# Performance work log

Measured on AMD Instinct MI355X. Metric: run time of the kernel, lower is better.

The kernel has to match this reference:

```python
import jax, jax.numpy as jnp
import numpy as np

BS = 64; T = 96; C = 16; IN = 16; H = 256; NH = 8; DH = H // NH
NCLS = 4; L = T + NCLS; LAYERS = 4; GDEP = 2; EPS = 1e-5


def _ln(x, g, b):
    m = x.mean(-1, keepdims=True)
    v = ((x - m) ** 2).mean(-1, keepdims=True)
    return (x - m) / jnp.sqrt(v + EPS) * g + b


def _mask():
    # causal upper-triangular -inf mask; last NCLS rows (cls tokens) attend everywhere
    m = jnp.where(jnp.triu(jnp.ones((L, L), jnp.float32), 1) > 0, -jnp.inf, 0.0)
    return m.at[-NCLS:].set(0.0)


def _enc(h, mask, Wqkv, bqkv, Wo, bo, W1, b1, W2, b2, g1, be1, g2, be2):
    # post-norm TransformerEncoderLayer (torch default), dropout=0
    B = h.shape[0]
    qkv = h @ Wqkv.T + bqkv
    q, k, v = jnp.split(qkv, 3, axis=-1)
    sp = lambda t: t.reshape(B, L, NH, DH).transpose(0, 2, 1, 3)
    q, k, v = sp(q), sp(k), sp(v)
    s = jnp.einsum('bhqd,bhkd->bhqk', q, k) / np.float32(np.sqrt(DH)) + mask
    a = jax.nn.softmax(s, axis=-1)
    o = jnp.einsum('bhqk,bhkd->bhqd', a, v).transpose(0, 2, 1, 3).reshape(B, L, H)
    h = _ln(h + o @ Wo.T + bo, g1, be1)
    ff = jax.nn.relu(h @ W1.T + b1) @ W2.T + b2
    return _ln(h + ff, g2, be2)


def _mixprop(x, g, Wm, bm):
    # x: (bs, H, C, NCLS); MTGNN mixprop with alpha=0
    adj = g + jnp.eye(C, dtype=g.dtype)
    a = adj / adj.sum(1, keepdims=True)
    h = x
    outs = [x]
    for _ in range(GDEP):
        h = jnp.einsum('ncwl,vw->ncvl', h, a)
        outs.append(h)
    ho = jnp.concatenate(outs, axis=1)  # (bs, (GDEP+1)*H, C, NCLS)
    return jnp.einsum('ncwl,oc->nowl', ho, Wm) + bm[None, :, None, None]


def _forward(x, Wfc, bfc, cls_token, pos_emb, emb1, emb2, Wl1, bl1, Wl2, bl2,
             Wqkv, bqkv, Wo, bo, W1, b1, W2, b2, ln1g, ln1b, ln2g, ln2b,
             Wmlp, bmlp, Wd1, bd1, Wd2, bd2):
    bs = x.shape[0]
    h = x @ Wfc.T + bfc                                      # (bs,T,C,H)
    h = jnp.concatenate([h, jnp.broadcast_to(cls_token, (bs, NCLS, C, H))], axis=1)
    h = h + pos_emb[None]                                    # (bs,L,C,H)
    h = jnp.swapaxes(h, 1, 2).reshape(bs * C, L, H)
    mask = _mask()
    # graph_constructor (alpha=1)
    m1 = jnp.tanh(emb1 @ Wl1.T + bl1)
    m2 = jnp.tanh(emb2 @ Wl2.T + bl2)
    g = jax.nn.relu(jnp.tanh(m1 @ m2.T - m2 @ m1.T))         # (C,C)
    h = _enc(h, mask, Wqkv[0], bqkv[0], Wo[0], bo[0], W1[0], b1[0], W2[0], b2[0],
             ln1g[0], ln1b[0], ln2g[0], ln2b[0])
    for l in range(1, LAYERS):
        cls = h[:, -NCLS:].reshape(bs, C, NCLS, H).transpose(0, 3, 1, 2)  # (bs,H,C,NCLS)
        cls = _mixprop(cls, g, Wmlp[l - 1], bmlp[l - 1])
        cls = cls.transpose(0, 2, 3, 1).reshape(bs * C, NCLS, H)
        h = jnp.concatenate([h[:, :-NCLS], cls], axis=1)
        h = _enc(h, mask, Wqkv[l], bqkv[l], Wo[l], bo[l], W1[l], b1[l], W2[l], b2[l],
                 ln1g[l], ln1b[l], ln2g[l], ln2b[l])
    z = jnp.tanh(h[:, -NCLS:].reshape(bs, C * NCLS * H))
    z = jax.nn.gelu(z @ Wd1.T + bd1, approximate=False) @ Wd2.T + bd2
    return z[:, 0]


def setup_inputs() -> dict:
    key = jax.random.key(0)
    ks = iter(jax.random.split(key, 64))
    rn = lambda *s: jax.random.normal(next(ks), s, dtype=jnp.float32) * 0.05
    d = {}
    d['x'] = jax.random.normal(next(ks), (BS, T, C, IN), dtype=jnp.float32)
    d['p'] = jnp.zeros((BS,), jnp.float32)
    d['y'] = jnp.zeros((BS,), jnp.float32)
    d['Wfc'] = rn(H, IN); d['bfc'] = jnp.zeros((H,), jnp.float32)
    d['cls_token'] = rn(1, NCLS, C, H) * 20.0  # torch randn scale ~1
    d['pos_emb'] = rn(NCLS + T, C, H) * 20.0
    d['emb1'] = rn(C, H); d['emb2'] = rn(C, H)
    d['Wl1'] = rn(H, H); d['bl1'] = jnp.zeros((H,), jnp.float32)
    d['Wl2'] = rn(H, H); d['bl2'] = jnp.zeros((H,), jnp.float32)
    d['Wqkv'] = rn(LAYERS, 3 * H, H); d['bqkv'] = jnp.zeros((LAYERS, 3 * H), jnp.float32)
    d['Wo'] = rn(LAYERS, H, H); d['bo'] = jnp.zeros((LAYERS, H), jnp.float32)
    d['W1'] = rn(LAYERS, 4 * H, H); d['b1'] = jnp.zeros((LAYERS, 4 * H), jnp.float32)
    d['W2'] = rn(LAYERS, H, 4 * H); d['b2'] = jnp.zeros((LAYERS, H), jnp.float32)
    d['ln1g'] = jnp.ones((LAYERS, H), jnp.float32); d['ln1b'] = jnp.zeros((LAYERS, H), jnp.float32)
    d['ln2g'] = jnp.ones((LAYERS, H), jnp.float32); d['ln2b'] = jnp.zeros((LAYERS, H), jnp.float32)
    d['Wmlp'] = rn(LAYERS - 1, H, (GDEP + 1) * H); d['bmlp'] = jnp.zeros((LAYERS - 1, H), jnp.float32)
    d['Wd1'] = rn(H, NCLS * C * H); d['bd1'] = jnp.zeros((H,), jnp.float32)
    d['Wd2'] = rn(1, H); d['bd2'] = jnp.zeros((1,), jnp.float32)
    return d


def reference(x, p, y, Wfc, bfc, cls_token, pos_emb, emb1, emb2, Wl1, bl1, Wl2, bl2,
              Wqkv, bqkv, Wo, bo, W1, b1, W2, b2, ln1g, ln1b, ln2g, ln2b,
              Wmlp, bmlp, Wd1, bd1, Wd2, bd2):
    # p, y are unused by the original forward (kept for signature parity)
    return _forward(x, Wfc, bfc, cls_token, pos_emb, emb1, emb2, Wl1, bl1, Wl2, bl2,
                    Wqkv, bqkv, Wo, bo, W1, b1, W2, b2, ln1g, ln1b, ln2g, ln2b,
                    Wmlp, bmlp, Wd1, bd1, Wd2, bd2)
```

## Files before the change

### kernel.cpp

```cpp
#include <hip/hip_runtime.h>
#include <hip/hip_bf16.h>
#include <math.h>

typedef unsigned short u16;
typedef unsigned int   u32;
typedef __attribute__((ext_vector_type(8))) short short8;
typedef __attribute__((ext_vector_type(4))) float f32x4;

#define BSZ   64
#define TT    96
#define CCH   16
#define INDIM 16
#define HD    256
#define NHEAD 8
#define DHEAD 32
#define NCLS  4
#define LSEQ  100
#define NLAY  4
#define EPSV  1e-5f
#define BSEQ  (BSZ*CCH)
#define MTOK  (BSEQ*LSEQ)

__device__ __forceinline__ float bf2f(u16 x){ return __uint_as_float(((u32)x)<<16); }
__device__ __forceinline__ u16 f2bf(float f){
    u32 u = __float_as_uint(f);
    u32 r = (u + 0x7fffu + ((u>>16)&1u)) >> 16;
    return (u16)r;
}
__device__ __forceinline__ float lo16(u32 r){ return __uint_as_float(r<<16); }
__device__ __forceinline__ float hi16(u32 r){ return __uint_as_float(r&0xffff0000u); }

__device__ __forceinline__ u32 cvtpk(float lo, float hi){
    u32 r;
    asm("v_cvt_pk_bf16_f32 %0, %1, %2" : "=v"(r) : "v"(lo), "v"(hi));
    return r;
}

__device__ __forceinline__ void gload_lds16(const u16* g, u16* l){
    __builtin_amdgcn_global_load_lds(
        (const __attribute__((address_space(1))) unsigned int*)g,
        (__attribute__((address_space(3))) unsigned int*)l, 16, 0, 0);
}

__global__ __launch_bounds__(256)
void k_cvt(const float* __restrict__ src, u16* __restrict__ dst, int n)
{
    for (int i = blockIdx.x*256 + threadIdx.x; i < n; i += gridDim.x*256)
        dst[i] = f2bf(src[i]);
}

__global__ __launch_bounds__(256)
void k_embed(const float* __restrict__ x, const float* __restrict__ Wfc,
             const float* __restrict__ bfc, const float* __restrict__ cls,
             const float* __restrict__ pos, u16* __restrict__ h)
{
    int s = blockIdx.x;
    int n = s >> 4, c = s & 15;
    int hc = threadIdx.x;
    float wr[INDIM];
    #pragma unroll
    for (int i=0;i<INDIM;i++) wr[i] = Wfc[hc*INDIM + i];
    float bb = bfc[hc];
    for (int l=0; l<TT; l++){
        const float* xr = x + (size_t)((n*TT + l)*CCH + c)*INDIM;
        float acc = bb;
        #pragma unroll
        for (int i=0;i<INDIM;i++) acc += xr[i]*wr[i];
        acc += pos[(size_t)(l*CCH + c)*HD + hc];
        h[((size_t)s*LSEQ + l)*HD + hc] = f2bf(acc);
    }
    #pragma unroll
    for (int l=TT; l<LSEQ; l++){
        float v = cls[(size_t)((l-TT)*CCH + c)*HD + hc]
                + pos[(size_t)(l*CCH + c)*HD + hc];
        h[((size_t)s*LSEQ + l)*HD + hc] = f2bf(v);
    }
}

__global__ __launch_bounds__(256)
void k_graph_m(const float* __restrict__ emb, const float* __restrict__ Wl,
               const float* __restrict__ bl, float* __restrict__ m)
{
    int r = blockIdx.x, o = threadIdx.x;
    __shared__ float e[HD];
    e[o] = emb[r*HD + o];
    __syncthreads();
    const float* w = Wl + (size_t)o*HD;
    float acc = bl[o];
    for (int k=0;k<HD;k++) acc += e[k]*w[k];
    m[r*HD + o] = tanhf(acc);
}

__global__ __launch_bounds__(256)
void k_graph_a(const float* __restrict__ m1, const float* __restrict__ m2,
               float* __restrict__ a)
{
    int t = threadIdx.x; int v = t >> 4, w = t & 15;
    __shared__ float adj[16][17];
    float s1=0.f, s2=0.f;
    for (int k=0;k<HD;k++){
        s1 += m1[v*HD+k]*m2[w*HD+k];
        s2 += m2[v*HD+k]*m1[w*HD+k];
    }
    float g = tanhf(s1 - s2); g = g > 0.f ? g : 0.f;
    adj[v][w] = g + (v==w ? 1.f : 0.f);
    __syncthreads();
    float rs = 0.f;
    #pragma unroll
    for (int j=0;j<16;j++) rs += adj[v][j];
    a[t] = adj[v][w] / rs;
}

__global__ __launch_bounds__(256)
void k_gemmA(const u16* __restrict__ A, int lda,
             const u16* __restrict__ W, const float* __restrict__ bias,
             u16* __restrict__ C, int ldc, int K, int relu, int scat)
{
    __shared__ u16 smem[32768];
    u16* As0 = smem;
    u16* As1 = smem + 8192;
    u16* Ws0 = smem + 16384;
    u16* Ws1 = smem + 24576;

    int t = threadIdx.x;
    int lane = t & 63, w = t >> 6;
    int wm = (w & 1)*64, wn = (w >> 1)*64;
    int fr = lane & 15, quad = lane >> 4;

    int nwg = gridDim.x * gridDim.y;
    int bid = blockIdx.y * gridDim.x + blockIdx.x;
    int tile = bid;
    if (!(nwg & 7)){
        int cpx = nwg >> 3;
        tile = (bid & 7)*cpx + (bid >> 3);
    }
    int bx = tile % gridDim.x, by = tile / gridDim.x;
    size_t mb = (size_t)by * 128;
    int nb = bx * 128;

    int srow = lane >> 2;
    int sslot = lane & 3;

    f32x4 acc[4][4] = {};

    auto STAGE = [&](int bb, int k0){
        #pragma unroll
        for (int i=0;i<2;i++){
            int r = w*32 + i*16 + srow;
            int cw = sslot ^ ((r>>1)&3);
            gload_lds16(&A[(mb + r)*(size_t)lda + k0      + cw*8], &As0[bb*4096 + (w*32 + i*16)*32]);
            gload_lds16(&A[(mb + r)*(size_t)lda + k0 + 32 + cw*8], &As1[bb*4096 + (w*32 + i*16)*32]);
            gload_lds16(&W[(size_t)(nb + r)*K   + k0      + cw*8], &Ws0[bb*4096 + (w*32 + i*16)*32]);
            gload_lds16(&W[(size_t)(nb + r)*K   + k0 + 32 + cw*8], &Ws1[bb*4096 + (w*32 + i*16)*32]);
        }
    };
    auto COMPUTE = [&](int bb){
        short8 af0[4], af1[4], bf0[4], bf1[4];
        #pragma unroll
        for (int mt=0; mt<4; mt++){
            int r = wm + mt*16 + fr;
            int sw = (quad ^ ((r>>1)&3)) << 3;
            af0[mt] = *(const short8*)&As0[bb*4096 + r*32 + sw];
            af1[mt] = *(const short8*)&As1[bb*4096 + r*32 + sw];
        }
        #pragma unroll
        for (int nt=0; nt<4; nt++){
            int r = wn + nt*16 + fr;
            int sw = (quad ^ ((r>>1)&3)) << 3;
            bf0[nt] = *(const short8*)&Ws0[bb*4096 + r*32 + sw];
            bf1[nt] = *(const short8*)&Ws1[bb*4096 + r*32 + sw];
        }
        #pragma unroll
        for (int mt=0; mt<4; mt++)
            #pragma unroll
            for (int nt=0; nt<4; nt++){
                acc[mt][nt] = __builtin_amdgcn_mfma_f32_16x16x32_bf16(
                    af0[mt], bf0[nt], acc[mt][nt], 0, 0, 0);
                acc[mt][nt] = __builtin_amdgcn_mfma_f32_16x16x32_bf16(
                    af1[mt], bf1[nt], acc[mt][nt], 0, 0, 0);
            }
    };

    const int nst = K >> 6;
    STAGE(0, 0);
    asm volatile("s_waitcnt vmcnt(0)" ::: "memory");
    __builtin_amdgcn_s_barrier();
    int b = 0;
    for (int ts = 0; ts < nst; ++ts){
        if (ts + 1 < nst) STAGE(b^1, (ts+1) << 6);
        COMPUTE(b);
        asm volatile("s_waitcnt vmcnt(0)" ::: "memory");
        __builtin_amdgcn_s_barrier();
        b ^= 1;
    }

    float bb4[4];
    #pragma unroll
    for (int nt=0; nt<4; nt++) bb4[nt] = bias[nb + wn + nt*16 + fr];
    __syncthreads();
    u16* Ct = smem;
    #pragma unroll
    for (int mt=0; mt<4; mt++){
        int rw = wm + mt*16 + quad*4;
        #pragma unroll
        for (int nt=0; nt<4; nt++){
            int col = wn + nt*16 + fr;
            float v0 = acc[mt][nt][0] + bb4[nt];
            float v1 = acc[mt][nt][1] + bb4[nt];
            float v2 = acc[mt][nt][2] + bb4[nt];
            float v3 = acc[mt][nt][3] + bb4[nt];
            if (relu){
                v0 = v0 > 0.f ? v0 : 0.f;  v1 = v1 > 0.f ? v1 : 0.f;
                v2 = v2 > 0.f ? v2 : 0.f;  v3 = v3 > 0.f ? v3 : 0.f;
            }
            u32 p01 = cvtpk(v0, v1), p23 = cvtpk(v2, v3);
            Ct[(rw+0)*128 + col] = (u16)p01;
            Ct[(rw+1)*128 + col] = (u16)(p01 >> 16);
            Ct[(rw+2)*128 + col] = (u16)p23;
            Ct[(rw+3)*128 + col] = (u16)(p23 >> 16);
        }
    }
    __syncthreads();
    #pragma unroll
    for (int it=0; it<8; ++it){
        int row = it*16 + (t>>4);
        int seg = t & 15;
        size_t rg = mb + row;
        if (scat) rg = (rg >> 2)*LSEQ + TT + (rg & 3);
        *(short8*)&C[rg*(size_t)ldc + nb + seg*8] = *(const short8*)&Ct[row*128 + seg*8];
    }
}

__global__ __launch_bounds__(256)
void k_gemmC(const u16* __restrict__ A, int lda, int K,
             const u16* __restrict__ W, const float* __restrict__ bias,
             u16* __restrict__ h, const float* __restrict__ gam,
             const float* __restrict__ bet, size_t row0)
{
    __shared__ u16 smem[40960];
    u16* As0 = smem;
    u16* As1 = smem + 4096;
    u16* Ws0 = smem + 8192;
    u16* Ws1 = smem + 24576;

    int t = threadIdx.x;
    int lane = t & 63, w = t >> 6;
    int fr = lane & 15, quad = lane >> 4;
    size_t mb = (size_t)blockIdx.x * 64;
    int srow = lane >> 2, sslot = lane & 3;

    f32x4 acc[4][4] = {};

    auto STAGE = [&](int bb, int k0){
        {
            int r = w*16 + srow;
            int cw = sslot ^ ((r>>1)&3);
            gload_lds16(&A[(mb + r)*(size_t)lda + k0      + cw*8], &As0[bb*2048 + (w*16)*32]);
            gload_lds16(&A[(mb + r)*(size_t)lda + k0 + 32 + cw*8], &As1[bb*2048 + (w*16)*32]);
        }
        #pragma unroll
        for (int i=0;i<4;i++){
            int r = w*64 + i*16 + srow;
            int cw = sslot ^ ((r>>1)&3);
            gload_lds16(&W[(size_t)r*K + k0      + cw*8], &Ws0[bb*8192 + (w*64 + i*16)*32]);
            gload_lds16(&W[(size_t)r*K + k0 + 32 + cw*8], &Ws1[bb*8192 + (w*64 + i*16)*32]);
        }
    };
    auto COMPUTE = [&](int bb){
        short8 af0[4], af1[4], bf0[4], bf1[4];
        #pragma unroll
        for (int mt=0; mt<4; mt++){
            int ra = mt*16 + fr;
            int swa = (quad ^ ((ra>>1)&3)) << 3;
            af0[mt] = *(const short8*)&As0[bb*2048 + ra*32 + swa];
            af1[mt] = *(const short8*)&As1[bb*2048 + ra*32 + swa];
        }
        #pragma unroll
        for (int nt=0; nt<4; nt++){
            int rb = w*64 + nt*16 + fr;
            int swb = (quad ^ ((rb>>1)&3)) << 3;
            bf0[nt] = *(const short8*)&Ws0[bb*8192 + rb*32 + swb];
            bf1[nt] = *(const short8*)&Ws1[bb*8192 + rb*32 + swb];
        }
        #pragma unroll
        for (int mt=0; mt<4; mt++)
            #pragma unroll
            for (int nt=0; nt<4; nt++){
                acc[mt][nt] = __builtin_amdgcn_mfma_f32_16x16x32_bf16(
                    af0[mt], bf0[nt], acc[mt][nt], 0, 0, 0);
                acc[mt][nt] = __builtin_amdgcn_mfma_f32_16x16x32_bf16(
                    af1[mt], bf1[nt], acc[mt][nt], 0, 0, 0);
            }
    };

    const int nst = K >> 6;
    STAGE(0, 0);
    asm volatile("s_waitcnt vmcnt(0)" ::: "memory");
    __builtin_amdgcn_s_barrier();
    int b = 0;
    for (int ts = 0; ts < nst; ++ts){
        if (ts + 1 < nst) STAGE(b^1, (ts+1) << 6);
        COMPUTE(b);
        asm volatile("s_waitcnt vmcnt(0)" ::: "memory");
        __builtin_amdgcn_s_barrier();
        b ^= 1;
    }

    float bb4[4], gg[4], be[4];
    #pragma unroll
    for (int nt=0; nt<4; nt++){
        int col = w*64 + nt*16 + fr;
        bb4[nt] = bias[col]; gg[nt] = gam[col]; be[nt] = bet[col];
    }
    #pragma unroll
    for (int mt=0; mt<4; mt++){
        #pragma unroll
        for (int r=0; r<4; r++){
            size_t row = row0 + mb + mt*16 + quad*4 + r;
            #pragma unroll
            for (int nt=0; nt<4; nt++)
                acc[mt][nt][r] += bb4[nt] + bf2f(h[row*HD + w*64 + nt*16 + fr]);
        }
    }
    __syncthreads();
    float* red  = (float*)smem;
    float* red2 = (float*)(smem + 512);
    float ps[4][4];
    #pragma unroll
    for (int mt=0; mt<4; mt++)
        #pragma unroll
        for (int r=0; r<4; r++){
            float s = acc[mt][0][r] + acc[mt][1][r] + acc[mt][2][r] + acc[mt][3][r];
            s += __shfl_xor(s,1,64); s += __shfl_xor(s,2,64);
            s += __shfl_xor(s,4,64); s += __shfl_xor(s,8,64);
            ps[mt][r] = s;
        }
    if (fr == 0){
        #pragma unroll
        for (int mt=0; mt<4; mt++)
            #pragma unroll
            for (int r=0; r<4; r++)
                red[w*64 + mt*16 + quad*4 + r] = ps[mt][r];
    }
    __syncthreads();
    float mean[4][4];
    #pragma unroll
    for (int mt=0; mt<4; mt++)
        #pragma unroll
        for (int r=0; r<4; r++){
            int rl = mt*16 + quad*4 + r;
            mean[mt][r] = (red[rl] + red[64+rl] + red[128+rl] + red[192+rl]) * (1.f/256.f);
            float s = 0.f;
            #pragma unroll
            for (int nt=0; nt<4; nt++){ float d = acc[mt][nt][r] - mean[mt][r]; s += d*d; }
            s += __shfl_xor(s,1,64); s += __shfl_xor(s,2,64);
            s += __shfl_xor(s,4,64); s += __shfl_xor(s,8,64);
            ps[mt][r] = s;
        }
    if (fr == 0){
        #pragma unroll
        for (int mt=0; mt<4; mt++)
            #pragma unroll
            for (int r=0; r<4; r++)
                red2[w*64 + mt*16 + quad*4 + r] = ps[mt][r];
    }
    __syncthreads();
    u16* Ct = smem + 8192;
    #pragma unroll
    for (int mt=0; mt<4; mt++)
        #pragma unroll
        for (int r=0; r<4; r++){
            int rl = mt*16 + quad*4 + r;
            float inv = rsqrtf((red2[rl] + red2[64+rl] + red2[128+rl] + red2[192+rl])
                               * (1.f/256.f) + EPSV);
            float o0 = (acc[mt][0][r] - mean[mt][r]) * inv * gg[0] + be[0];
            float o1 = (acc[mt][1][r] - mean[mt][r]) * inv * gg[1] + be[1];
            float o2 = (acc[mt][2][r] - mean[mt][r]) * inv * gg[2] + be[2];
            float o3 = (acc[mt][3][r] - mean[mt][r]) * inv * gg[3] + be[3];
            u32 p01 = cvtpk(o0, o1), p23 = cvtpk(o2, o3);
            Ct[rl*256 + w*64 +  0 + fr] = (u16)p01;
            Ct[rl*256 + w*64 + 16 + fr] = (u16)(p01 >> 16);
            Ct[rl*256 + w*64 + 32 + fr] = (u16)p23;
            Ct[rl*256 + w*64 + 48 + fr] = (u16)(p23 >> 16);
        }
    __syncthreads();
    #pragma unroll
    for (int it=0; it<8; ++it){
        int row = it*8 + (t>>5);
        int seg = t & 31;
        *(short8*)&h[(row0 + mb + row)*HD + seg*8] = *(const short8*)&Ct[row*256 + seg*8];
    }
}

#define KS_STR 40
#define VT_STR 136
#define PL_STR 136
__global__ __launch_bounds__(256)
void k_attn(u16* __restrict__ qkv)
{
    __shared__ u16 smem[26368];
    int t = threadIdx.x;
    int w = t >> 6, lane = t & 63;
    int fr = lane & 15, quad = lane >> 4;
    int p = t >> 7, t2 = t & 127;
    u16* Ks = smem + p*4480;
    u16* Vt = smem + 8960 + p*4352;
    u16* Pl = smem + 17664 + w*2176;

    {
        int gp = blockIdx.x*2 + p;
        size_t base = (size_t)(gp >> 3)*LSEQ*768 + (gp & 7)*32;
        for (int idx = t2; idx < 1792; idx += 128){
            int key = idx >> 4, d2 = (idx & 15) << 1;
            u32 kv = (key < LSEQ) ? *(const u32*)&qkv[base + (size_t)key*768 + 256 + d2] : 0u;
            *(u32*)&Ks[key*KS_STR + d2] = kv;
        }
        for (int idx = t2; idx < 2048; idx += 128){
            int key = idx >> 4, d2 = (idx & 15) << 1;
            u32 vv = (key < LSEQ) ? *(const u32*)&qkv[base + (size_t)key*768 + 512 + d2] : 0u;
            Vt[ d2   *VT_STR + key] = (u16)(vv & 0xffffu);
            Vt[(d2+1)*VT_STR + key] = (u16)(vv >> 16);
        }
    }
    __syncthreads();

    int wp = w >> 1;
    int gp = blockIdx.x*2 + wp;
    size_t base = (size_t)(gp >> 3)*LSEQ*768 + (gp & 7)*32;
    u16* Ksw = smem + wp*4480;
    u16* Vtw = smem + 8960 + wp*4352;

    short8 kf[7];
    #pragma unroll
    for (int nt=0; nt<7; nt++)
        kf[nt] = *(const short8*)&Ksw[(nt*16 + fr)*KS_STR + quad*8];
    short8 vfr[4][2];
    #pragma unroll
    for (int ks=0; ks<4; ks++)
        #pragma unroll
        for (int nt=0; nt<2; nt++)
            vfr[ks][nt] = *(const short8*)&Vtw[(nt*16 + fr)*VT_STR + ks*32 + quad*8];

    const float scale = 0.17677669529663687f;
    int smask = (w & 1) ? 0x34 : 0x4B;
    #pragma unroll
    for (int st = 0; st < 7; ++st){
        if (!((smask >> st) & 1)) continue;
        const int ntile = (st == 6) ? 7 : (st + 1);
        const int nks   = (st == 6) ? 4 : (st/2 + 1);
        int q = st*16 + fr;
        short8 qf = {};
        if (q < LSEQ) qf = *(const short8*)&qkv[base + (size_t)q*768 + quad*8];
        f32x4 S[7];
        #pragma unroll
        for (int nt=0; nt<7; nt++){
            if (nt >= ntile) continue;
            f32x4 z = {};
            S[nt] = __builtin_amdgcn_mfma_f32_16x16x32_bf16(qf, kf[nt], z, 0,0,0);
        }
        float mx[4] = {-1e30f,-1e30f,-1e30f,-1e30f};
        #pragma unroll
        for (int r=0;r<4;r++){
            int qr = st*16 + quad*4 + r;
            int jmax = (qr < TT) ? qr : (LSEQ-1);
            #pragma unroll
            for (int nt=0;nt<7;nt++){
                if (nt >= ntile) continue;
                int j = nt*16 + fr;
                float s = (j <= jmax) ? S[nt][r]*scale : -1e30f;
                S[nt][r] = s;
                mx[r] = fmaxf(mx[r], s);
            }
        }
        #pragma unroll
        for (int r=0;r<4;r++){
            #pragma unroll
            for (int m=1;m<16;m<<=1) mx[r] = fmaxf(mx[r], __shfl_xor(mx[r], m, 64));
        }
        float l4[4] = {0.f,0.f,0.f,0.f};
        #pragma unroll
        for (int r=0;r<4;r++){
            #pragma unroll
            for (int nt=0;nt<7;nt++){
                if (nt >= ntile) continue;
                float pv = __expf(S[nt][r] - mx[r]);
                S[nt][r] = pv;
                l4[r] += pv;
            }
        }
        #pragma unroll
        for (int r=0;r<4;r++){
            #pragma unroll
            for (int m=1;m<16;m<<=1) l4[r] += __shfl_xor(l4[r], m, 64);
        }
        #pragma unroll
        for (int nt=0;nt<7;nt++){
            if (nt >= ntile) continue;
            #pragma unroll
            for (int r=0;r<4;r++){
                u16 hb = f2bf(S[nt][r]);
                Pl[(quad*4+r)*PL_STR + nt*16 + fr] = hb;
                S[nt][r] -= bf2f(hb);
            }
        }
        if (ntile*16 < nks*32){
            #pragma unroll
            for (int r=0;r<4;r++)
                Pl[(quad*4+r)*PL_STR + ntile*16 + fr] = 0;
        }
        __builtin_amdgcn_s_waitcnt(0);
        f32x4 D[2] = {};
        #pragma unroll
        for (int ks=0; ks<4; ks++){
            if (ks >= nks) continue;
            short8 pf = *(const short8*)&Pl[fr*PL_STR + ks*32 + quad*8];
            #pragma unroll
            for (int nt=0; nt<2; nt++)
                D[nt] = __builtin_amdgcn_mfma_f32_16x16x32_bf16(pf, vfr[ks][nt], D[nt], 0,0,0);
        }
        __builtin_amdgcn_s_waitcnt(0);
        #pragma unroll
        for (int nt=0;nt<7;nt++){
            if (nt >= ntile) continue;
            #pragma unroll
            for (int r=0;r<4;r++)
                Pl[(quad*4+r)*PL_STR + nt*16 + fr] = f2bf(S[nt][r]);
        }
        __builtin_amdgcn_s_waitcnt(0);
        #pragma unroll
        for (int ks=0; ks<4; ks++){
            if (ks >= nks) continue;
            short8 pf = *(const short8*)&Pl[fr*PL_STR + ks*32 + quad*8];
            #pragma unroll
            for (int nt=0; nt<2; nt++)
                D[nt] = __builtin_amdgcn_mfma_f32_16x16x32_bf16(pf, vfr[ks][nt], D[nt], 0,0,0);
        }
        #pragma unroll
        for (int r=0;r<4;r++){
            int qr = st*16 + quad*4 + r;
            if (qr < LSEQ){
                float inv = 1.f / l4[r];
                #pragma unroll
                for (int nt=0; nt<2; nt++)
                    qkv[base + (size_t)qr*768 + nt*16 + fr] = f2bf(D[nt][r]*inv);
            }
        }
        __builtin_amdgcn_s_waitcnt(0);
    }
}

__global__ __launch_bounds__(256)
void k_mixprep(const u16* __restrict__ h, const float* __restrict__ a,
               u16* __restrict__ amid)
{
    int n = blockIdx.x >> 2, tt = blockIdx.x & 3;
    __shared__ float xs[256][17], h1s[256][17], h2s[256][17];
    __shared__ float as[16][17];
    int t = threadIdx.x;
    as[t>>4][t&15] = a[t];
    for (int idx=t; idx<4096; idx+=256){
        int w = idx >> 8, hc = idx & 255;
        xs[hc][w] = bf2f(h[((size_t)(n*16 + w)*LSEQ + TT + tt)*HD + hc]);
    }
    __syncthreads();
    for (int idx=t; idx<4096; idx+=256){
        int v = idx & 15, hc = idx >> 4;
        float acc = 0.f;
        #pragma unroll
        for (int w=0;w<16;w++) acc += as[v][w]*xs[hc][w];
        h1s[hc][v] = acc;
    }
    __syncthreads();
    for (int idx=t; idx<4096; idx+=256){
        int v = idx & 15, hc = idx >> 4;
        float acc = 0.f;
        #pragma unroll
        for (int w=0;w<16;w++) acc += as[v][w]*h1s[hc][w];
        h2s[hc][v] = acc;
    }
    __syncthreads();
    int hc = t;
    #pragma unroll
    for (int w=0;w<16;w++){
        size_t row = (size_t)((n*16 + w)*4 + tt);
        amid[row*768 +       hc] = f2bf(xs[hc][w]);
        amid[row*768 + 256 + hc] = f2bf(h1s[hc][w]);
        amid[row*768 + 512 + hc] = f2bf(h2s[hc][w]);
    }
}

__global__ __launch_bounds__(256)
void k_z(const u16* __restrict__ h, u16* __restrict__ z)
{
    int bid = blockIdx.x, t = threadIdx.x;
    #pragma unroll
    for (int tc=0;tc<4;tc++)
        z[((size_t)bid*4 + tc)*HD + t] = f2bf(tanhf(bf2f(h[((size_t)bid*LSEQ + TT + tc)*HD + t])));
}

__global__ __launch_bounds__(256)
void k_head1p(const u16* __restrict__ z, const float* __restrict__ Wd1,
              float* __restrict__ d1p)
{
    __shared__ float zch[64][137];
    __shared__ float wt[16][137];
    int t = threadIdx.x;
    int col = t & 15, rgrp = t >> 4;
    int ob = blockIdx.x * 16;
    int kb = blockIdx.y;
    float acc[4] = {0.f,0.f,0.f,0.f};
    for (int kc=0; kc<1024; kc+=128){
        int base_k = kb*1024 + kc;
        #pragma unroll
        for (int jj=0; jj<16; jj++){
            int idx = t + jj*256;
            int n = idx >> 6, k2 = (idx & 63) << 1;
            u32 r = *(const u32*)&z[(size_t)n*16384 + base_k + k2];
            zch[n][k2] = lo16(r); zch[n][k2+1] = hi16(r);
        }
        #pragma unroll
        for (int jj=0; jj<2; jj++){
            int idx = t + jj*256;
            int r = idx >> 5, k4 = (idx & 31) << 2;
            float4 w4 = *(const float4*)&Wd1[(size_t)(ob + r)*16384 + base_k + k4];
            wt[r][k4] = w4.x; wt[r][k4+1] = w4.y; wt[r][k4+2] = w4.z; wt[r][k4+3] = w4.w;
        }
        __syncthreads();
        for (int k=0;k<128;k++){
            float wv = wt[col][k];
            #pragma unroll
            for (int u=0;u<4;u++) acc[u] += zch[rgrp + 16*u][k]*wv;
        }
        __syncthreads();
    }
    #pragma unroll
    for (int u=0;u<4;u++)
        d1p[(size_t)(kb*64 + rgrp + 16*u)*HD + ob + col] = acc[u];
}

__global__ __launch_bounds__(256)
void k_headf(const float* __restrict__ d1p, const float* __restrict__ bd1,
             const float* __restrict__ Wd2, const float* __restrict__ bd2,
             float* __restrict__ out)
{
    __shared__ float red[4];
    int n = blockIdx.x, c = threadIdx.x;
    float s = 0.f;
    #pragma unroll
    for (int kb=0; kb<16; kb++) s += d1p[(size_t)(kb*64 + n)*HD + c];
    float xx = s + bd1[c];
    float ge = 0.5f*xx*(1.f + erff(xx*0.70710678118654752f));
    float p = ge * Wd2[c];
    #pragma unroll
    for (int m=1;m<64;m<<=1) p += __shfl_xor(p, m, 64);
    if ((c & 63) == 0) red[c >> 6] = p;
    __syncthreads();
    if (c == 0) out[n] = red[0]+red[1]+red[2]+red[3] + bd2[0];
}

extern "C" void kernel_launch(void* const* d_in, const int* in_sizes, int n_in,
                              void* d_out, int out_size, void* d_ws, size_t ws_size,
                              hipStream_t stream)
{
    const float* x    = (const float*)d_in[0];
    const float* Wfc  = (const float*)d_in[3];
    const float* bfc  = (const float*)d_in[4];
    const float* cls  = (const float*)d_in[5];
    const float* pos  = (const float*)d_in[6];
    const float* emb1 = (const float*)d_in[7];
    const float* emb2 = (const float*)d_in[8];
    const float* Wl1  = (const float*)d_in[9];
    const float* bl1  = (const float*)d_in[10];
    const float* Wl2  = (const float*)d_in[11];
    const float* bl2  = (const float*)d_in[12];
    const float* Wqkv = (const float*)d_in[13];
    const float* bqkv = (const float*)d_in[14];
    const float* Wo   = (const float*)d_in[15];
    const float* bo   = (const float*)d_in[16];
    const float* W1   = (const float*)d_in[17];
    const float* b1   = (const float*)d_in[18];
    const float* W2   = (const float*)d_in[19];
    const float* b2   = (const float*)d_in[20];
    const float* ln1g = (const float*)d_in[21];
    const float* ln1b = (const float*)d_in[22];
    const float* ln2g = (const float*)d_in[23];
    const float* ln2b = (const float*)d_in[24];
    const float* Wmlp = (const float*)d_in[25];
    const float* bmlp = (const float*)d_in[26];
    const float* Wd1  = (const float*)d_in[27];
    const float* bd1  = (const float*)d_in[28];
    const float* Wd2  = (const float*)d_in[29];
    const float* bd2  = (const float*)d_in[30];

    int NCH = 8;
    {
        const size_t fixed = 63145088 + (1<<20);
        if      (fixed + (size_t)MTOK    *2560 <= ws_size) NCH = 1;
        else if (fixed + (size_t)(MTOK/2)*2560 <= ws_size) NCH = 2;
        else if (fixed + (size_t)(MTOK/4)*2560 <= ws_size) NCH = 4;
    }
    const int RCH = MTOK / NCH;
    const int SCH = BSEQ / NCH;

    u16* h    = (u16*)d_ws;
    u16* buf  = h    + (size_t)MTOK*HD;
    u16* buf2 = buf  + (size_t)RCH*1024;
    u16* wq   = buf2 + (size_t)RCH*256;
    u16* wo   = wq   + (size_t)4*768*256;
    u16* w1   = wo   + (size_t)4*256*256;
    u16* w2   = w1   + (size_t)4*1024*256;
    u16* wmb  = w2   + (size_t)4*256*1024;
    u16* zb   = wmb  + (size_t)3*256*768;
    float* fp = (float*)(zb + (size_t)BSZ*16384);
    float* m1  = fp;
    float* m2  = m1 + CCH*HD;
    float* an  = m2 + CCH*HD;
    float* d1p = an + CCH*CCH;

    k_cvt<<<512, 256, 0, stream>>>(Wqkv, wq, 4*768*256);
    k_cvt<<<256, 256, 0, stream>>>(Wo,   wo, 4*256*256);
    k_cvt<<<512, 256, 0, stream>>>(W1,   w1, 4*1024*256);
    k_cvt<<<512, 256, 0, stream>>>(W2,   w2, 4*256*1024);
    k_cvt<<<256, 256, 0, stream>>>(Wmlp, wmb, 3*256*768);

    k_embed<<<BSEQ, 256, 0, stream>>>(x, Wfc, bfc, cls, pos, h);
    k_graph_m<<<16, 256, 0, stream>>>(emb1, Wl1, bl1, m1);
    k_graph_m<<<16, 256, 0, stream>>>(emb2, Wl2, bl2, m2);
    k_graph_a<<<1, 256, 0, stream>>>(m1, m2, an);

    for (int l=0; l<NLAY; l++){
        if (l > 0){
            k_mixprep<<<BSZ*NCLS, 256, 0, stream>>>(h, an, buf);
            k_gemmA<<<dim3(256/128, 4096/128), 256, 0, stream>>>(
                buf, 768, wmb + (size_t)(l-1)*256*768, bmlp + (size_t)(l-1)*HD,
                h, HD, 768, 0, 1);
        }

        for (int c=0; c<NCH; c++){
            size_t row0 = (size_t)c * RCH;
            k_gemmA<<<dim3(768/128, RCH/128), 256, 0, stream>>>(
                h + row0*HD, HD, wq + (size_t)l*768*256, bqkv + (size_t)l*768,
                buf, 768, HD, 0, 0);
            k_attn<<<SCH*NHEAD/2, 256, 0, stream>>>(buf);
            k_gemmC<<<RCH/64, 256, 0, stream>>>(
                buf, 768, HD, wo + (size_t)l*256*256, bo + (size_t)l*HD,
                h, ln1g + (size_t)l*HD, ln1b + (size_t)l*HD, row0);
            k_gemmA<<<dim3(1024/128, RCH/128), 256, 0, stream>>>(
                h + row0*HD, HD, w1 + (size_t)l*1024*256, b1 + (size_t)l*1024,
                buf, 1024, HD, 1, 0);
            k_gemmC<<<RCH/64, 256, 0, stream>>>(
                buf, 1024, 1024, w2 + (size_t)l*256*1024, b2 + (size_t)l*HD,
                h, ln2g + (size_t)l*HD, ln2b + (size_t)l*HD, row0);
        }
    }

    k_z<<<BSZ*CCH, 256, 0, stream>>>(h, zb);
    k_head1p<<<dim3(16, 16), 256, 0, stream>>>(zb, Wd1, d1p);
    k_headf<<<BSZ, 256, 0, stream>>>(d1p, bd1, Wd2, bd2, (float*)d_out);
}
```

Measured before the change: 2.104 ms.

## Restructure attention P staging with swizzled hi/lo buffers and preloaded Q

Preloads all Q fragments before a barrier so the K smem region can be reused. The hi and lo bf16 parts of P are then written to two separate XOR-swizzled LDS buffers in a single pass instead of two sequential write/read rounds. It also changes the V transpose load order to reduce bank conflicts and replaces full waitcnt(0) with lgkmcnt-only waits. The cost is more registers for the seven Q fragments and an extra block-wide sync.

```diff
diff --git a/kernel.cpp b/kernel.cpp
--- a/kernel.cpp
+++ b/kernel.cpp
@@ -394,7 +394,6 @@
 
 #define KS_STR 40
 #define VT_STR 136
-#define PL_STR 136
 __global__ __launch_bounds__(256)
 void k_attn(u16* __restrict__ qkv)
 {
@@ -405,7 +404,6 @@
     int p = t >> 7, t2 = t & 127;
     u16* Ks = smem + p*4480;
     u16* Vt = smem + 8960 + p*4352;
-    u16* Pl = smem + 17664 + w*2176;
 
     {
         int gp = blockIdx.x*2 + p;
@@ -416,7 +414,7 @@
             *(u32*)&Ks[key*KS_STR + d2] = kv;
         }
         for (int idx = t2; idx < 2048; idx += 128){
-            int key = idx >> 4, d2 = (idx & 15) << 1;
+            int key = idx & 127, d2 = (idx >> 7) << 1;
             u32 vv = (key < LSEQ) ? *(const u32*)&qkv[base + (size_t)key*768 + 512 + d2] : 0u;
             Vt[ d2   *VT_STR + key] = (u16)(vv & 0xffffu);
             Vt[(d2+1)*VT_STR + key] = (u16)(vv >> 16);
@@ -441,22 +439,32 @@
         for (int nt=0; nt<2; nt++)
             vfr[ks][nt] = *(const short8*)&Vtw[(nt*16 + fr)*VT_STR + ks*32 + quad*8];
 
+    const int smask = (w & 1) ? 0x34 : 0x4B;
+    short8 qfs[7];
+    #pragma unroll
+    for (int st=0; st<7; ++st){
+        if (!((smask >> st) & 1)) continue;
+        int q = st*16 + fr;
+        short8 z = {};
+        qfs[st] = (q < LSEQ) ? *(const short8*)&qkv[base + (size_t)q*768 + quad*8] : z;
+    }
+    __syncthreads();
+
+    u16* Ph = smem + w*2048;
+    u16* Pv = smem + 17664 + w*2048;
+
     const float scale = 0.17677669529663687f;
-    int smask = (w & 1) ? 0x34 : 0x4B;
     #pragma unroll
     for (int st = 0; st < 7; ++st){
         if (!((smask >> st) & 1)) continue;
         const int ntile = (st == 6) ? 7 : (st + 1);
         const int nks   = (st == 6) ? 4 : (st/2 + 1);
-        int q = st*16 + fr;
-        short8 qf = {};
-        if (q < LSEQ) qf = *(const short8*)&qkv[base + (size_t)q*768 + quad*8];
         f32x4 S[7];
         #pragma unroll
         for (int nt=0; nt<7; nt++){
             if (nt >= ntile) continue;
             f32x4 z = {};
-            S[nt] = __builtin_amdgcn_mfma_f32_16x16x32_bf16(qf, kf[nt], z, 0,0,0);
+            S[nt] = __builtin_amdgcn_mfma_f32_16x16x32_bf16(qfs[st], kf[nt], z, 0,0,0);
         }
         float mx[4] = {-1e30f,-1e30f,-1e30f,-1e30f};
         #pragma unroll
@@ -493,47 +501,41 @@
             #pragma unroll
             for (int m=1;m<16;m<<=1) l4[r] += __shfl_xor(l4[r], m, 64);
         }
+        asm volatile("s_waitcnt lgkmcnt(0)" ::: "memory");
         #pragma unroll
         for (int nt=0;nt<7;nt++){
             if (nt >= ntile) continue;
             #pragma unroll
             for (int r=0;r<4;r++){
+                int row = quad*4 + r;
+                int a = (nt>>1)*512 + row*32 + ((((nt&1)<<4) + fr) ^ ((((row)>>1)&3)<<3));
                 u16 hb = f2bf(S[nt][r]);
-                Pl[(quad*4+r)*PL_STR + nt*16 + fr] = hb;
-                S[nt][r] -= bf2f(hb);
+                Ph[a] = hb;
+                Pv[a] = f2bf(S[nt][r] - bf2f(hb));
             }
         }
         if (ntile*16 < nks*32){
             #pragma unroll
-            for (int r=0;r<4;r++)
-                Pl[(quad*4+r)*PL_STR + ntile*16 + fr] = 0;
-        }
-        __builtin_amdgcn_s_waitcnt(0);
+            for (int r=0;r<4;r++){
+                int row = quad*4 + r;
+                int a = (ntile>>1)*512 + row*32 + ((((ntile&1)<<4) + fr) ^ ((((row)>>1)&3)<<3));
+                Ph[a] = 0;
+                Pv[a] = 0;
+            }
+        }
+        asm volatile("s_waitcnt lgkmcnt(0)" ::: "memory");
         f32x4 D[2] = {};
         #pragma unroll
         for (int ks=0; ks<4; ks++){
             if (ks >= nks) continue;
-            short8 pf = *(const short8*)&Pl[fr*PL_STR + ks*32 + quad*8];
-            #pragma unroll
-            for (int nt=0; nt<2; nt++)
-                D[nt] = __builtin_amdgcn_mfma_f32_16x16x32_bf16(pf, vfr[ks][nt], D[nt], 0,0,0);
-        }
-        __builtin_amdgcn_s_waitcnt(0);
-        #pragma unroll
-        for (int nt=0;nt<7;nt++){
-            if (nt >= ntile) continue;
-            #pragma unroll
-            for (int r=0;r<4;r++)
-                Pl[(quad*4+r)*PL_STR + nt*16 + fr] = f2bf(S[nt][r]);
-        }
-        __builtin_amdgcn_s_waitcnt(0);
-        #pragma unroll
-        for (int ks=0; ks<4; ks++){
-            if (ks >= nks) continue;
-            short8 pf = *(const short8*)&Pl[fr*PL_STR + ks*32 + quad*8];
-            #pragma unroll
-            for (int nt=0; nt<2; nt++)
-                D[nt] = __builtin_amdgcn_mfma_f32_16x16x32_bf16(pf, vfr[ks][nt], D[nt], 0,0,0);
+            int a = ks*512 + fr*32 + ((quad ^ ((fr>>1)&3)) << 3);
+            short8 ph = *(const short8*)&Ph[a];
+            short8 pl = *(const short8*)&Pv[a];
+            #pragma unroll
+            for (int nt=0; nt<2; nt++){
+                D[nt] = __builtin_amdgcn_mfma_f32_16x16x32_bf16(ph, vfr[ks][nt], D[nt], 0,0,0);
+                D[nt] = __builtin_amdgcn_mfma_f32_16x16x32_bf16(pl, vfr[ks][nt], D[nt], 0,0,0);
+            }
         }
         #pragma unroll
         for (int r=0;r<4;r++){
@@ -545,7 +547,6 @@
                     qkv[base + (size_t)qr*768 + nt*16 + fr] = f2bf(D[nt][r]*inv);
             }
         }
-        __builtin_amdgcn_s_waitcnt(0);
     }
 }
 
```

Measured after the change: 2.127 ms. No clear change (+1.1%).
